# Kernel optimization log

Measured on AMD Instinct MI355X. Metric: run time of the kernel, lower is better.

Reference implementation:

```python
import jax, jax.numpy as jnp
import numpy as np

B, T, F, H, FC = 32, 2048, 128, 512, 128


def setup_inputs() -> dict:
    key = jax.random.key(0)
    ks = jax.random.split(key, 10)
    x = jax.random.normal(ks[0], (B, T, F), dtype=jnp.float32)
    lengths = jax.random.randint(ks[1], (B,), 1, T + 1)
    s = 1.0 / np.sqrt(H)  # torch nn.RNN init: U(-1/sqrt(hidden), 1/sqrt(hidden))
    W_ih = jax.random.uniform(ks[2], (H, F), jnp.float32, -s, s)
    W_hh = jax.random.uniform(ks[3], (H, H), jnp.float32, -s, s)
    b_ih = jax.random.uniform(ks[4], (H,), jnp.float32, -s, s)
    b_hh = jax.random.uniform(ks[5], (H,), jnp.float32, -s, s)
    s1 = 1.0 / np.sqrt(H)
    W1 = jax.random.uniform(ks[6], (FC, H), jnp.float32, -s1, s1)
    b1 = jax.random.uniform(ks[7], (FC,), jnp.float32, -s1, s1)
    s2 = 1.0 / np.sqrt(FC)
    W2 = jax.random.uniform(ks[8], (1, FC), jnp.float32, -s2, s2)
    b2 = jax.random.uniform(ks[9], (1,), jnp.float32, -s2, s2)
    return {"x": x, "lengths": lengths, "W_ih": W_ih, "W_hh": W_hh,
            "b_ih": b_ih, "b_hh": b_hh, "W1": W1, "b1": b1, "W2": W2, "b2": b2}


def reference(x, lengths, W_ih, W_hh, b_ih, b_hh, W1, b1, W2, b2):
    # x: [B, T, F] padded ragged sequences; lengths: [B]
    Bs, Ts, Fs = x.shape
    Hs = W_ih.shape[0]
    mask = jnp.arange(Ts)[None, :] < lengths[:, None]          # [B, T]
    xs = (jnp.swapaxes(x, 0, 1), mask.T)                       # time-major [T, B, ...]

    def step(h, inp):
        x_t, m_t = inp
        # vanilla RNN cell: h' = tanh(W_ih x + b_ih + W_hh h + b_hh)
        h_new = jnp.tanh(x_t @ W_ih.T + b_ih + h @ W_hh.T + b_hh)
        h = jnp.where(m_t[:, None], h_new, h)                  # freeze hidden past seq end
        return h, h_new

    h0 = jnp.zeros((Bs, Hs), dtype=x.dtype)
    h_final, outp = jax.lax.scan(step, h0, xs)                 # h_final [B,H], outp [T,B,H]

    # fcn: Linear(H,128) -> Linear(128,1) -> ReLU, applied to every timestep output
    n = jax.nn.relu((outp @ W1.T + b1) @ W2.T + b2)            # [T, B, 1]
    pos = (n[..., 0] > 0) & mask.T                             # count only valid timesteps
    outs = jnp.sum(pos, axis=0).astype(jnp.float32)[:, None]   # [B, 1]
    return outs, h_final
```

## Files before the change

### kernel.cpp

```cpp
#include <hip/hip_runtime.h>
#include <math.h>
#include <stdint.h>

#define BB 32
#define TT 2048
#define FF 128
#define HH 512
#define FCC 128
#define QW 8
#define NTH 640

#define SCALE_F     4194304.0f
#define INV_SCALE_F (1.0f/4194304.0f)
#define CNT_ONE     (1ull<<48)
#define BIAS_TOTAL  (1ll<<46)
#define BIAS_SHARE  (1ll<<43)

typedef float f32x2 __attribute__((ext_vector_type(2)));

__global__ void ws_zero(uint64_t* g) {
    g[(size_t)blockIdx.x * blockDim.x + threadIdx.x] = 0ull;
}

__device__ __forceinline__ void wait_lgkm0() {
    asm volatile("s_waitcnt lgkmcnt(0)" ::: "memory");
}

__device__ __forceinline__ float fast_tanh(float z) {
    float ax = fabsf(z);
    float e  = __expf(-2.0f * ax);
    float r  = (1.0f - e) / (1.0f + e);
    return copysignf(r, z);
}

__device__ __forceinline__ void pk_fma(f32x2& d, f32x2 a, f32x2 b) {
    asm("v_pk_fma_f32 %0, %1, %2, %0" : "+v"(d) : "v"(a), "v"(b));
}
__device__ __forceinline__ f32x2 lo2(float4 v) { f32x2 r; r.x = v.x; r.y = v.y; return r; }
__device__ __forceinline__ f32x2 hi2(float4 v) { f32x2 r; r.x = v.z; r.y = v.w; return r; }

__device__ __forceinline__ uint64_t gld_agent(const uint64_t* p) {
    return __hip_atomic_load(p, __ATOMIC_RELAXED, __HIP_MEMORY_SCOPE_AGENT);
}
__device__ __forceinline__ int flag_ld(const int* p) {
    return __hip_atomic_load(p, __ATOMIC_RELAXED, __HIP_MEMORY_SCOPE_WORKGROUP);
}

__global__ __launch_bounds__(NTH, 1)
void rnn_seq(const float* __restrict__ x, const int* __restrict__ lengths,
             const float* __restrict__ W_ih, const float* __restrict__ W_hh,
             const float* __restrict__ b_ih, const float* __restrict__ b_hh,
             const float* __restrict__ W1, const float* __restrict__ b1,
             const float* __restrict__ W2, const float* __restrict__ b2,
             float* __restrict__ out, uint64_t* __restrict__ ws)
{
    const int blk  = blockIdx.x;
    const int b    = blk >> 3;
    const int q    = blk & 7;
    const int tid  = threadIdx.x;
    const int w    = tid >> 6;
    const int lane = tid & 63;
    const int len  = lengths[b];

    uint64_t* gh  = ws;
    uint64_t* gsd = ws + 2 * BB * HH;

    __shared__ float hsh[2][64];
    __shared__ float biass[64];
    __shared__ int   flag_s;

    if (w == 8) {
        biass[lane] = b_ih[q * 64 + lane] + b_hh[q * 64 + lane];
        hsh[0][lane] = 0.0f;
        if (lane == 0) flag_s = 0;
    }
    __syncthreads();

    if (w < 8) {
        const int r = w * 64 + lane;
        float4 ww[16];
        { const float4* p = (const float4*)(W_hh + (size_t)r * HH + q * 64);
          #pragma unroll
          for (int k = 0; k < 16; ++k) ww[k] = p[k]; }
        float4 wi[4];
        { const float4* p = (const float4*)(W_ih + r * FF + q * 16);
          #pragma unroll
          for (int k = 0; k < 4; ++k) wi[k] = p[k]; }
        float wvreg = 0.0f;
        if (w == 7) {
            const int col = q * 64 + lane;
            #pragma unroll 8
            for (int f = 0; f < FCC; ++f) wvreg += W2[f] * W1[f * HH + col];
        }
        int prevI[2] = {0, 0};
        const float* xb = x + (size_t)b * TT * FF + q * 16;
        float4 xc[4], xn[4];
        { const float4* p = (const float4*)xb;
          #pragma unroll
          for (int k = 0; k < 4; ++k) xc[k] = p[k]; }
        { const float4* p = (const float4*)(xb + FF);
          #pragma unroll
          for (int k = 0; k < 4; ++k) xn[k] = p[k]; }

        uint64_t* ghb = gh + (size_t)b * HH + r;

        for (int i = 0; i < len; ++i) {
            f32x2 acc01 = {0.0f, 0.0f};
            f32x2 acc23 = {0.0f, 0.0f};
            #pragma unroll
            for (int k = 0; k < 4; ++k) {
                pk_fma(acc01, lo2(wi[k]), lo2(xc[k]));
                pk_fma(acc23, hi2(wi[k]), hi2(xc[k]));
            }

            {
                int f0 = flag_ld(&flag_s);
                int f1 = flag_ld(&flag_s);
                for (;;) {
                    if (f0 >= i) break;
                    f0 = flag_ld(&flag_s);
                    if (f1 >= i) break;
                    f1 = flag_ld(&flag_s);
                }
            }
            const float* hc = hsh[i & 1];
            const float4* hq = (const float4*)hc;
            #pragma unroll
            for (int k = 0; k < 16; ++k) {
                float4 hk = hq[k];
                pk_fma(acc01, lo2(ww[k]), lo2(hk));
                pk_fma(acc23, hi2(ww[k]), hi2(hk));
            }
            float A = (acc01.x + acc01.y) + (acc23.x + acc23.y);

            float hown = 0.0f;
            if (w == 7) hown = hc[lane];

            int fi = __float2int_rn(A * SCALE_F);
            const int pn = (i + 1) & 1;
            long long con = (long long)CNT_ONE + (long long)(fi - prevI[pn])
                          + ((i < 2) ? BIAS_SHARE : 0);
            prevI[pn] = fi;
            atomicAdd((unsigned long long*)(ghb + (size_t)pn * BB * HH),
                      (unsigned long long)con);

            if (w == 7 && i > 0) {
                float d = hown * wvreg;
                d += __shfl_xor(d, 1);  d += __shfl_xor(d, 2);
                d += __shfl_xor(d, 4);  d += __shfl_xor(d, 8);
                d += __shfl_xor(d, 16); d += __shfl_xor(d, 32);
                if (lane == 0) {
                    uint64_t pk = ((uint64_t)(uint32_t)i << 32) |
                                  (uint64_t)__float_as_uint(d);
                    __hip_atomic_store(&gsd[((size_t)b * 16 + (i & 15)) * 8 + q],
                                       pk, __ATOMIC_RELAXED, __HIP_MEMORY_SCOPE_AGENT);
                }
            }
            #pragma unroll
            for (int k = 0; k < 4; ++k) xc[k] = xn[k];
            if (i + 2 < len) {
                const float4* p = (const float4*)(xb + (size_t)(i + 2) * FF);
                #pragma unroll
                for (int k = 0; k < 4; ++k) xn[k] = p[k];
            }
        }
        if (w == 7) {
            while (flag_ld(&flag_s) < len) {}
            float d = hsh[len & 1][lane] * wvreg;
            d += __shfl_xor(d, 1);  d += __shfl_xor(d, 2);
            d += __shfl_xor(d, 4);  d += __shfl_xor(d, 8);
            d += __shfl_xor(d, 16); d += __shfl_xor(d, 32);
            if (lane == 0) {
                uint64_t pk = ((uint64_t)(uint32_t)len << 32) |
                              (uint64_t)__float_as_uint(d);
                __hip_atomic_store(&gsd[((size_t)b * 16 + (len & 15)) * 8 + q],
                                   pk, __ATOMIC_RELAXED, __HIP_MEMORY_SCOPE_AGENT);
            }
        }
    } else if (w == 8) {
        __builtin_amdgcn_s_setprio(1);
        float hval = 0.0f;
        for (int i = 0; i < len; ++i) {
            const int j  = i + 1;
            const int pn = j & 1;
            const uint64_t target = 8ull * (uint64_t)((j + 1) >> 1);
            uint64_t* pr = gh + (size_t)pn * BB * HH + (size_t)b * HH + q * 64 + lane;
            uint64_t u;
            uint64_t u0 = gld_agent(pr);
            uint64_t u1 = gld_agent(pr);
            uint64_t u2 = gld_agent(pr);
            uint64_t u3 = gld_agent(pr);
            for (;;) {
                if (__all((u0 >> 48) == target)) { u = u0; break; }
                u0 = gld_agent(pr);
                if (__all((u1 >> 48) == target)) { u = u1; break; }
                u1 = gld_agent(pr);
                if (__all((u2 >> 48) == target)) { u = u2; break; }
                u2 = gld_agent(pr);
                if (__all((u3 >> 48) == target)) { u = u3; break; }
                u3 = gld_agent(pr);
            }
            float pre = (float)(int)(uint32_t)u * INV_SCALE_F + biass[lane];
            hval = fast_tanh(pre);
            hsh[pn][lane] = hval;
            wait_lgkm0();
            if (lane == 0)
                __hip_atomic_store(&flag_s, j, __ATOMIC_RELAXED,
                                   __HIP_MEMORY_SCOPE_WORKGROUP);
        }
        out[BB + b * HH + q * 64 + lane] = hval;
    } else {
        if (q != 0) return;
        float cconst = b2[0];
        for (int f = 0; f < FCC; ++f) cconst += W2[f] * b1[f];
        int count = 0;
        for (int j = 1; j <= len; ++j) {
            float d = 0.0f;
            if (lane < 8) {
                uint64_t* pr = gsd + ((size_t)b * 16 + (j & 15)) * 8 + lane;
                uint64_t u;
                do { u = gld_agent(pr); }
                while ((int)(u >> 32) != j);
                d = __uint_as_float((uint32_t)u);
            }
            d += __shfl_xor(d, 1); d += __shfl_xor(d, 2); d += __shfl_xor(d, 4);
            if (lane == 0 && d + cconst > 0.0f) ++count;
        }
        if (lane == 0) out[b] = (float)count;
    }
}

extern "C" void kernel_launch(void* const* d_in, const int* in_sizes, int n_in,
                              void* d_out, int out_size, void* d_ws, size_t ws_size,
                              hipStream_t stream) {
    const float* x    = (const float*)d_in[0];
    const int*   lens = (const int*)d_in[1];
    const float* W_ih = (const float*)d_in[2];
    const float* W_hh = (const float*)d_in[3];
    const float* b_ih = (const float*)d_in[4];
    const float* b_hh = (const float*)d_in[5];
    const float* W1   = (const float*)d_in[6];
    const float* b1   = (const float*)d_in[7];
    const float* W2   = (const float*)d_in[8];
    const float* b2   = (const float*)d_in[9];
    float* out = (float*)d_out;
    uint64_t* ws = (uint64_t*)d_ws;

    ws_zero<<<dim3(144), dim3(256), 0, stream>>>(ws);
    rnn_seq<<<dim3(BB * QW), dim3(NTH), 0, stream>>>(
        x, lens, W_ih, W_hh, b_ih, b_hh, W1, b1, W2, b2, out, ws);
}
```

Baseline: 3.172 ms.

## Detect same-XCD co-location and use workgroup-scope atomics for the cross-block exchange

The block-to-batch mapping changes so the 8 blocks of one sequence are spread as blk&31 / blk>>5, which is meant to make it likely they land on the same XCD. At startup each block reads its XCC ID and a per-batch counter records which XCDs its peers landed on. If all 8 sit on one XCD, the hidden-state exchange uses workgroup-scope atomics (L2-local) instead of agent-scope ones, cutting cross-die coherence latency on the per-step critical path. The unrolled multi-load polling loops are also simplified to single-load spins. The risk is a startup barrier across blocks, plus a fallback path if the hardware scheduler does not place the blocks as hoped.

```diff
diff --git a/kernel.cpp b/kernel.cpp
--- a/kernel.cpp
+++ b/kernel.cpp
@@ -16,10 +16,13 @@
 #define BIAS_TOTAL  (1ll<<46)
 #define BIAS_SHARE  (1ll<<43)
 
+#define WS_U64 (2*BB*HH + BB*16*8 + BB)
+
 typedef float f32x2 __attribute__((ext_vector_type(2)));
 
 __global__ void ws_zero(uint64_t* g) {
-    g[(size_t)blockIdx.x * blockDim.x + threadIdx.x] = 0ull;
+    size_t i = (size_t)blockIdx.x * blockDim.x + threadIdx.x;
+    if (i < WS_U64) g[i] = 0ull;
 }
 
 __device__ __forceinline__ void wait_lgkm0() {
@@ -55,8 +58,8 @@
              float* __restrict__ out, uint64_t* __restrict__ ws)
 {
     const int blk  = blockIdx.x;
-    const int b    = blk >> 3;
-    const int q    = blk & 7;
+    const int b    = blk & 31;
+    const int q    = blk >> 5;
     const int tid  = threadIdx.x;
     const int w    = tid >> 6;
     const int lane = tid & 63;
@@ -64,17 +67,32 @@
 
     uint64_t* gh  = ws;
     uint64_t* gsd = ws + 2 * BB * HH;
+    uint64_t* gx  = gsd + BB * 16 * 8;
 
     __shared__ float hsh[2][64];
     __shared__ float biass[64];
     __shared__ int   flag_s;
+    __shared__ int   lok_s;
 
     if (w == 8) {
         biass[lane] = b_ih[q * 64 + lane] + b_hh[q * 64 + lane];
         hsh[0][lane] = 0.0f;
-        if (lane == 0) flag_s = 0;
+        uint32_t xcc_raw;
+        asm volatile("s_getreg_b32 %0, hwreg(HW_REG_XCC_ID)" : "=s"(xcc_raw));
+        const uint32_t xcc = xcc_raw & 7;
+        if (lane == 0) {
+            flag_s = 0;
+            uint64_t* gxp = gx + b;
+            __hip_atomic_fetch_add(gxp, 1ull << (8 * xcc),
+                                   __ATOMIC_RELAXED, __HIP_MEMORY_SCOPE_AGENT);
+            uint64_t v;
+            do { v = gld_agent(gxp); }
+            while ((uint8_t)((v * 0x0101010101010101ull) >> 56) != 8);
+            lok_s = (v == (8ull << (8 * xcc))) ? 1 : 0;
+        }
     }
     __syncthreads();
+    const bool lok = (lok_s != 0);
 
     if (w < 8) {
         const int r = w * 64 + lane;
@@ -113,16 +131,7 @@
                 pk_fma(acc23, hi2(wi[k]), hi2(xc[k]));
             }
 
-            {
-                int f0 = flag_ld(&flag_s);
-                int f1 = flag_ld(&flag_s);
-                for (;;) {
-                    if (f0 >= i) break;
-                    f0 = flag_ld(&flag_s);
-                    if (f1 >= i) break;
-                    f1 = flag_ld(&flag_s);
-                }
-            }
+            while (flag_ld(&flag_s) < i) {}
             const float* hc = hsh[i & 1];
             const float4* hq = (const float4*)hc;
             #pragma unroll
@@ -141,8 +150,12 @@
             long long con = (long long)CNT_ONE + (long long)(fi - prevI[pn])
                           + ((i < 2) ? BIAS_SHARE : 0);
             prevI[pn] = fi;
-            atomicAdd((unsigned long long*)(ghb + (size_t)pn * BB * HH),
-                      (unsigned long long)con);
+            uint64_t* slot = ghb + (size_t)pn * BB * HH;
+            if (lok)
+                __hip_atomic_fetch_add(slot, (uint64_t)con,
+                                       __ATOMIC_RELAXED, __HIP_MEMORY_SCOPE_WORKGROUP);
+            else
+                atomicAdd((unsigned long long*)slot, (unsigned long long)con);
 
             if (w == 7 && i > 0) {
                 float d = hown * wvreg;
@@ -179,6 +192,8 @@
         }
     } else if (w == 8) {
         __builtin_amdgcn_s_setprio(1);
+        uint64_t z = 0;
+        asm("" : "+v"(z));
         float hval = 0.0f;
         for (int i = 0; i < len; ++i) {
             const int j  = i + 1;
@@ -186,19 +201,12 @@
             const uint64_t target = 8ull * (uint64_t)((j + 1) >> 1);
             uint64_t* pr = gh + (size_t)pn * BB * HH + (size_t)b * HH + q * 64 + lane;
             uint64_t u;
-            uint64_t u0 = gld_agent(pr);
-            uint64_t u1 = gld_agent(pr);
-            uint64_t u2 = gld_agent(pr);
-            uint64_t u3 = gld_agent(pr);
-            for (;;) {
-                if (__all((u0 >> 48) == target)) { u = u0; break; }
-                u0 = gld_agent(pr);
-                if (__all((u1 >> 48) == target)) { u = u1; break; }
-                u1 = gld_agent(pr);
-                if (__all((u2 >> 48) == target)) { u = u2; break; }
-                u2 = gld_agent(pr);
-                if (__all((u3 >> 48) == target)) { u = u3; break; }
-                u3 = gld_agent(pr);
+            if (lok) {
+                do { u = __hip_atomic_fetch_add(pr, z, __ATOMIC_RELAXED,
+                                                __HIP_MEMORY_SCOPE_WORKGROUP); }
+                while ((u >> 48) != target);
+            } else {
+                do { u = gld_agent(pr); } while ((u >> 48) != target);
             }
             float pre = (float)(int)(uint32_t)u * INV_SCALE_F + biass[lane];
             hval = fast_tanh(pre);
@@ -246,7 +254,7 @@
     float* out = (float*)d_out;
     uint64_t* ws = (uint64_t*)d_ws;
 
-    ws_zero<<<dim3(144), dim3(256), 0, stream>>>(ws);
+    ws_zero<<<dim3(145), dim3(256), 0, stream>>>(ws);
     rnn_seq<<<dim3(BB * QW), dim3(NTH), 0, stream>>>(
         x, lens, W_ih, W_hh, b_ih, b_hh, W1, b1, W2, b2, out, ws);
 }
```

Result: faster. 2.767 ms (-12.8%).
